# Kernel optimization log

Measured on AMD Instinct MI355X. Metric: run time of the kernel, lower is better.

The kernel has to match this reference:

```python
import jax, jax.numpy as jnp
import numpy as np

NUM_HEADS = 16
EPS = 1e-06


def setup_inputs() -> dict:
    key = jax.random.key(0)
    ks = jax.random.split(key, 6)
    b, s, d = 4, 4096, 1024
    scale = 1.0 / np.sqrt(d)
    return {
        "x": jax.random.normal(ks[0], (b, s, d), dtype=jnp.float32),
        "wq": jax.random.normal(ks[1], (d, d), dtype=jnp.float32) * scale,
        "wk": jax.random.normal(ks[2], (d, d), dtype=jnp.float32) * scale,
        "wv": jax.random.normal(ks[3], (d, d), dtype=jnp.float32) * scale,
        "wo": jax.random.normal(ks[4], (d, d), dtype=jnp.float32) * scale,
        "bo": jnp.zeros((d,), dtype=jnp.float32),
    }


def _split_heads(t, h):
    b, s, d = t.shape
    return t.reshape(b, s, h, d // h).transpose(0, 2, 1, 3)  # [b,h,s,dh]


def reference(x, wq, wk, wv, wo, bo):
    h = NUM_HEADS
    # torch Linear: y = x @ W.T (no bias for q/k/v)
    q = _split_heads(x @ wq.T, h)
    k = _split_heads(x @ wk.T, h)
    v = _split_heads(x @ wv.T, h)
    # ELU+1 feature map
    qf = jax.nn.elu(q) + 1.0
    kf = jax.nn.elu(k) + 1.0
    # global key feature sum over sequence: [b,h,dh]
    k_sum = jnp.sum(kf, axis=-2)
    # denominator: [b,h,s,1]
    denom = jnp.sum(qf * k_sum[:, :, None, :], axis=-1, keepdims=True) + EPS
    # kv = sum_s kf_s (outer) v_s  -> [b,h,dh,dh]  (the broadcast-sum in torch == matmul)
    kv = jnp.einsum('bhsd,bhse->bhde', kf, v)
    # q_kv: [b,h,s,dh]
    q_kv = jnp.einsum('bhsd,bhde->bhse', qf, kv)
    out = q_kv / denom
    b, _, s, dh = out.shape
    out = out.transpose(0, 2, 1, 3).reshape(b, s, h * dh)  # merge heads
    return out @ wo.T + bo
```

## Files before the change

kernel.cpp:

```cpp
#include <hip/hip_runtime.h>
#include <hip/hip_bf16.h>
#include <cmath>


#define TOK    16384
#define DMODEL 1024
#define NHEAD  16
#define DH     64
#define KSPLIT 8

using bf16x8 = __attribute__((ext_vector_type(8))) short;
using f32x4  = __attribute__((ext_vector_type(4))) float;

typedef __attribute__((address_space(1))) const unsigned int gld_src_t;
typedef __attribute__((address_space(3))) unsigned int gld_dst_t;

__device__ __forceinline__ unsigned short f2bf(float x) {
    unsigned int u = __float_as_uint(x);
    u += 0x7fffu + ((u >> 16) & 1u);
    return (unsigned short)(u >> 16);
}
__device__ __forceinline__ float bf2f(unsigned short b) {
    return __uint_as_float((unsigned int)b << 16);
}

__global__ __launch_bounds__(256) void split_k(
    const float* __restrict__ in, unsigned short* __restrict__ hi,
    unsigned short* __restrict__ lo, int n)
{
    int i = (blockIdx.x * 256 + threadIdx.x) * 4;
    if (i >= n) return;
    float4 v = *(const float4*)(in + i);
    float vs[4] = {v.x, v.y, v.z, v.w};
    unsigned short hh[4], ll[4];
#pragma unroll
    for (int j = 0; j < 4; ++j) {
        unsigned short h = f2bf(vs[j]);
        hh[j] = h;
        ll[j] = f2bf(vs[j] - bf2f(h));
    }
    *(ushort4*)(hi + i) = make_ushort4(hh[0], hh[1], hh[2], hh[3]);
    *(ushort4*)(lo + i) = make_ushort4(ll[0], ll[1], ll[2], ll[3]);
}

__global__ __launch_bounds__(256) void splitw_k(
    const float* __restrict__ w0, const float* __restrict__ w1,
    const float* __restrict__ w2, const float* __restrict__ w3,
    unsigned short* __restrict__ hs, unsigned short* __restrict__ ls)
{
    int w = blockIdx.x >> 10;
    const float* src = (w == 0) ? w0 : (w == 1) ? w1 : (w == 2) ? w2 : w3;
    int i = ((blockIdx.x & 1023) * 256 + threadIdx.x) * 4;
    size_t base = (size_t)w * (DMODEL * DMODEL);
    float4 v = *(const float4*)(src + i);
    float vs[4] = {v.x, v.y, v.z, v.w};
    unsigned short hh[4], ll[4];
#pragma unroll
    for (int j = 0; j < 4; ++j) {
        unsigned short h = f2bf(vs[j]);
        hh[j] = h;
        ll[j] = f2bf(vs[j] - bf2f(h));
    }
    *(ushort4*)(hs + base + i) = make_ushort4(hh[0], hh[1], hh[2], hh[3]);
    *(ushort4*)(ls + base + i) = make_ushort4(ll[0], ll[1], ll[2], ll[3]);
}

template<int ACT>
__global__ __launch_bounds__(512, 2) void gemm256_k(
    const unsigned short* __restrict__ Ah, const unsigned short* __restrict__ Al,
    const unsigned short* __restrict__ Bh, const unsigned short* __restrict__ Bl,
    const float* __restrict__ bias, float* __restrict__ C,
    int M, int N, int K)
{
    __shared__ unsigned short lds[2][4][256 * 32];
    const int tid  = threadIdx.x;
    const int lane = tid & 63, wid = tid >> 6;

    const int nwg = gridDim.x, cpx = nwg >> 3;
    const int g = ((int)blockIdx.x & 7) * cpx + ((int)blockIdx.x >> 3);
    const int m0 = (g >> 2) * 256, n0 = (g & 3) * 256;

    const int wr = wid >> 2, wc = wid & 3;
    const int fr = lane & 15, ko = lane >> 4;

    f32x4 acc[8][4];
#pragma unroll
    for (int i = 0; i < 8; ++i)
#pragma unroll
        for (int j = 0; j < 4; ++j) acc[i][j] = (f32x4){0.f, 0.f, 0.f, 0.f};

    const unsigned short* srcb = (wid < 2) ? Ah : (wid < 4) ? Al : (wid < 6) ? Bh : Bl;
    const int rowbase = ((wid < 4) ? m0 : n0) + (wid & 1) * 128;
    const int rloc = (wid & 1) * 128 + (lane >> 2);
    const int sslot = (lane & 3) ^ ((rloc >> 1) & 3);
    const unsigned short* gsrc0 = srcb + (size_t)(rowbase + (lane >> 2)) * K + sslot * 8;
    const int mat  = wid >> 1;
    const int ldso = ((wid & 1) * 128) * 32;

    const int koff = (ko ^ ((fr >> 1) & 3)) * 8;

    const int nt = K / 32;

#pragma unroll
    for (int t = 0; t < 8; ++t) {
        __builtin_amdgcn_global_load_lds((gld_src_t*)(gsrc0 + (size_t)t * 16 * K),
            (gld_dst_t*)&lds[0][mat][ldso + t * 512], 16, 0, 0);
    }
    __syncthreads();

    for (int t = 0; t < nt; ++t) {
        const int cur = t & 1;
        if (t + 1 < nt) {
            const unsigned short* gk = gsrc0 + (size_t)(t + 1) * 32;
#pragma unroll
            for (int u = 0; u < 8; ++u) {
                __builtin_amdgcn_global_load_lds((gld_src_t*)(gk + (size_t)u * 16 * K),
                    (gld_dst_t*)&lds[cur ^ 1][mat][ldso + u * 512], 16, 0, 0);
            }
        }
        bf16x8 ah[8], al[8];
#pragma unroll
        for (int mi = 0; mi < 8; ++mi) {
            int off = (wr * 128 + mi * 16 + fr) * 32 + koff;
            ah[mi] = *(const bf16x8*)&lds[cur][0][off];
            al[mi] = *(const bf16x8*)&lds[cur][1][off];
        }
#pragma unroll
        for (int nj = 0; nj < 4; ++nj) {
            int off = (wc * 64 + nj * 16 + fr) * 32 + koff;
            bf16x8 bh = *(const bf16x8*)&lds[cur][2][off];
            bf16x8 bl = *(const bf16x8*)&lds[cur][3][off];
#pragma unroll
            for (int mi = 0; mi < 8; ++mi) {
                acc[mi][nj] = __builtin_amdgcn_mfma_f32_16x16x32_bf16(ah[mi], bh, acc[mi][nj], 0, 0, 0);
                acc[mi][nj] = __builtin_amdgcn_mfma_f32_16x16x32_bf16(ah[mi], bl, acc[mi][nj], 0, 0, 0);
                acc[mi][nj] = __builtin_amdgcn_mfma_f32_16x16x32_bf16(al[mi], bh, acc[mi][nj], 0, 0, 0);
            }
        }
        __syncthreads();
    }

    const int fq = ko;
#pragma unroll
    for (int mi = 0; mi < 8; ++mi) {
#pragma unroll
        for (int i = 0; i < 4; ++i) {
            int m = m0 + wr * 128 + mi * 16 + fq * 4 + i;
            float* crow = C + (size_t)m * N + n0 + wc * 64;
#pragma unroll
            for (int nj = 0; nj < 4; ++nj) {
                int n = nj * 16 + fr;
                float v = acc[mi][nj][i];
                if (ACT == 1) v = (v > 0.f) ? (v + 1.f) : expf(v);
                if (ACT == 2) v += bias[n0 + wc * 64 + n];
                crow[n] = v;
            }
        }
    }
}

__global__ __launch_bounds__(256) void kv_partial_k(
    const float* __restrict__ kf, const float* __restrict__ vchunk,
    int bh_base, float* __restrict__ kvp, float* __restrict__ ksp)
{
    __shared__ float kfs[8][64];
    __shared__ float vs[8][64];
    const int bh = bh_base + blockIdx.x;
    const int split = blockIdx.y;
    const int b = bh >> 4, h = bh & 15;
    const int blocal = b - (bh_base >> 4);
    const int tid = threadIdx.x;
    const int col = tid & 63, rg = tid >> 6;
    const int tx = tid & 15, ty = tid >> 4;
    const int di0 = ty * 4, dj0 = tx * 4;

    float acc[4][4] = {};
    float ks[4] = {0.f, 0.f, 0.f, 0.f};

    const int rows = 4096 / KSPLIT;
    const size_t kbase = ((size_t)b * 4096 + (size_t)split * rows) * DMODEL + h * DH;
    const size_t vbase = ((size_t)blocal * 4096 + (size_t)split * rows) * DMODEL + h * DH;

    for (int it = 0; it < rows / 8; ++it) {
        __syncthreads();
#pragma unroll
        for (int p = 0; p < 2; ++p) {
            int r = rg + p * 4;
            size_t o = (size_t)(it * 8 + r) * DMODEL + col;
            kfs[r][col] = kf[kbase + o];
            vs[r][col]  = vchunk[vbase + o];
        }
        __syncthreads();
#pragma unroll
        for (int r = 0; r < 8; ++r) {
            float a[4], bb[4];
#pragma unroll
            for (int i = 0; i < 4; ++i) a[i] = kfs[r][di0 + i];
#pragma unroll
            for (int j = 0; j < 4; ++j) bb[j] = vs[r][dj0 + j];
#pragma unroll
            for (int i = 0; i < 4; ++i)
#pragma unroll
                for (int j = 0; j < 4; ++j)
                    acc[i][j] = fmaf(a[i], bb[j], acc[i][j]);
            if (tx == 0) {
#pragma unroll
                for (int i = 0; i < 4; ++i) ks[i] += a[i];
            }
        }
    }

    const size_t obase = ((size_t)(bh * KSPLIT + split)) * (DH * DH);
#pragma unroll
    for (int i = 0; i < 4; ++i)
#pragma unroll
        for (int j = 0; j < 4; ++j)
            kvp[obase + (size_t)(di0 + i) * DH + dj0 + j] = acc[i][j];
    if (tx == 0) {
        size_t kb = ((size_t)(bh * KSPLIT + split)) * DH + di0;
#pragma unroll
        for (int i = 0; i < 4; ++i) ksp[kb + i] = ks[i];
    }
}

__global__ __launch_bounds__(256) void reduce_kv_k(
    const float* __restrict__ kvp, const float* __restrict__ ksp,
    float* __restrict__ kv, float* __restrict__ ksum)
{
    int idx = blockIdx.x * 256 + threadIdx.x;
    int bh = idx >> 12, off = idx & 4095;
    float s = 0.f;
    for (int c = 0; c < KSPLIT; ++c) s += kvp[((size_t)(bh * KSPLIT + c)) * 4096 + off];
    kv[idx] = s;
    if (idx < 64 * DH) {
        int bh2 = idx >> 6, o2 = idx & 63;
        float t = 0.f;
        for (int c = 0; c < KSPLIT; ++c) t += ksp[((size_t)(bh2 * KSPLIT + c)) * DH + o2];
        ksum[idx] = t;
    }
}

__global__ __launch_bounds__(256) void attn_out_k(
    const float* __restrict__ qf_in, const float* __restrict__ kv,
    const float* __restrict__ ksum, unsigned short* __restrict__ out_hi,
    unsigned short* __restrict__ out_lo)
{
    __shared__ float kvs[DH * DH];
    __shared__ float qfs[16][DH];
    __shared__ float ksums[DH];
    __shared__ float denoms[16];
    const int hh = blockIdx.y;
    const int t0 = blockIdx.x * 16;
    const int b = t0 >> 12;
    const int bh = b * NHEAD + hh;
    const int tid = threadIdx.x;

    for (int i = tid; i < DH * DH; i += 256) kvs[i] = kv[(size_t)bh * (DH * DH) + i];
    for (int i = tid; i < 16 * DH; i += 256) {
        int tok = i >> 6, e = i & 63;
        qfs[tok][e] = qf_in[(size_t)(t0 + tok) * DMODEL + hh * DH + e];
    }
    if (tid < DH) ksums[tid] = ksum[(size_t)bh * DH + tid];
    __syncthreads();
    if (tid < 16) {
        float d = 0.f;
#pragma unroll
        for (int i = 0; i < DH; ++i) d += qfs[tid][i] * ksums[i];
        denoms[tid] = d + 1e-6f;
    }
    __syncthreads();
#pragma unroll
    for (int k = 0; k < 4; ++k) {
        int o = tid + k * 256;
        int tok = o >> 6, e = o & 63;
        float s = 0.f;
#pragma unroll
        for (int d = 0; d < DH; ++d) s = fmaf(qfs[tok][d], kvs[d * DH + e], s);
        s /= denoms[tok];
        size_t idx = (size_t)(t0 + tok) * DMODEL + hh * DH + e;
        unsigned short hb = f2bf(s);
        out_hi[idx] = hb;
        out_lo[idx] = f2bf(s - bf2f(hb));
    }
}

extern "C" void kernel_launch(void* const* d_in, const int* in_sizes, int n_in,
                              void* d_out, int out_size, void* d_ws, size_t ws_size,
                              hipStream_t stream)
{
    const float* x  = (const float*)d_in[0];
    const float* wq = (const float*)d_in[1];
    const float* wk = (const float*)d_in[2];
    const float* wv = (const float*)d_in[3];
    const float* wo = (const float*)d_in[4];
    const float* bo = (const float*)d_in[5];
    float* out = (float*)d_out;

    const size_t XE = (size_t)TOK * DMODEL;
    const size_t WE = (size_t)DMODEL * DMODEL;
    const size_t CE = (size_t)8192 * DMODEL;

    unsigned short* xh = (unsigned short*)d_ws;
    unsigned short* xl = xh + XE;
    unsigned short* wh = xl + XE;
    unsigned short* wl = wh + 4 * WE;
    float* kf   = (float*)(wl + 4 * WE);
    float* vc   = kf + XE;
    float* kvp  = vc + CE;
    float* ksp  = kvp + (size_t)64 * KSPLIT * DH * DH;
    float* kvb  = ksp + (size_t)64 * KSPLIT * DH;
    float* ksmb = kvb + (size_t)64 * DH * DH;
    float* qf   = kf;

    split_k<<<(int)(XE / 1024), 256, 0, stream>>>(x, xh, xl, (int)XE);
    splitw_k<<<4096, 256, 0, stream>>>(wq, wk, wv, wo, wh, wl);

    const int gfull = (TOK / 256) * 4;
    const int ghalf = (8192 / 256) * 4;

    gemm256_k<1><<<gfull, 512, 0, stream>>>(xh, xl, wh + WE, wl + WE, nullptr, kf, TOK, DMODEL, DMODEL);

    gemm256_k<0><<<ghalf, 512, 0, stream>>>(xh, xl, wh + 2 * WE, wl + 2 * WE, nullptr, vc, 8192, DMODEL, DMODEL);
    kv_partial_k<<<dim3(32, KSPLIT), 256, 0, stream>>>(kf, vc, 0, kvp, ksp);

    gemm256_k<0><<<ghalf, 512, 0, stream>>>(xh + CE, xl + CE, wh + 2 * WE, wl + 2 * WE, nullptr, vc, 8192, DMODEL, DMODEL);
    kv_partial_k<<<dim3(32, KSPLIT), 256, 0, stream>>>(kf, vc, 32, kvp, ksp);

    reduce_kv_k<<<dim3(64 * DH * DH / 256), 256, 0, stream>>>(kvp, ksp, kvb, ksmb);

    gemm256_k<1><<<gfull, 512, 0, stream>>>(xh, xl, wh, wl, nullptr, qf, TOK, DMODEL, DMODEL);
    attn_out_k<<<dim3(TOK / 16, NHEAD), 256, 0, stream>>>(qf, kvb, ksmb, xh, xl);

    gemm256_k<2><<<gfull, 512, 0, stream>>>(xh, xl, wh + 3 * WE, wl + 3 * WE, bo, out, TOK, DMODEL, DMODEL);
}
```

Baseline: 585.0 us.

## Compute attention output with split-bf16 MFMA, folding denominator into augmented KV

The Q projection GEMM now writes its feature-mapped output directly as hi/lo bf16 pairs instead of fp32. The KV reduction emits a transposed, bf16-split KV matrix with k_sum appended as extra rows. A new MFMA-based attention kernel then computes q·kv and the denominator in one pass of 3-term split-bf16 matrix products. This replaces the scalar fp32 FMA attention kernel and halves the Q intermediate traffic, at the cost of bf16x3 rounding in the attention step and some padding rows in the KV tile.

New measurement: 523.7 us, median of 2. 1.12x faster.

```diff
diff --git a/kernel.cpp b/kernel.cpp
--- a/kernel.cpp
+++ b/kernel.cpp
@@ -70,6 +70,7 @@
     const unsigned short* __restrict__ Ah, const unsigned short* __restrict__ Al,
     const unsigned short* __restrict__ Bh, const unsigned short* __restrict__ Bl,
     const float* __restrict__ bias, float* __restrict__ C,
+    unsigned short* __restrict__ Ch, unsigned short* __restrict__ Cl,
     int M, int N, int K)
 {
     __shared__ unsigned short lds[2][4][256 * 32];
@@ -98,7 +99,6 @@
     const int ldso = ((wid & 1) * 128) * 32;
 
     const int koff = (ko ^ ((fr >> 1) & 3)) * 8;
-
     const int nt = K / 32;
 
 #pragma unroll
@@ -146,14 +146,20 @@
 #pragma unroll
         for (int i = 0; i < 4; ++i) {
             int m = m0 + wr * 128 + mi * 16 + fq * 4 + i;
-            float* crow = C + (size_t)m * N + n0 + wc * 64;
+            size_t rbase = (size_t)m * N + n0 + wc * 64;
 #pragma unroll
             for (int nj = 0; nj < 4; ++nj) {
                 int n = nj * 16 + fr;
                 float v = acc[mi][nj][i];
-                if (ACT == 1) v = (v > 0.f) ? (v + 1.f) : expf(v);
+                if (ACT == 1 || ACT == 3) v = (v > 0.f) ? (v + 1.f) : expf(v);
                 if (ACT == 2) v += bias[n0 + wc * 64 + n];
-                crow[n] = v;
+                if (ACT == 3) {
+                    unsigned short hb = f2bf(v);
+                    Ch[rbase + n] = hb;
+                    Cl[rbase + n] = f2bf(v - bf2f(hb));
+                } else {
+                    C[rbase + n] = v;
+                }
             }
         }
     }
@@ -225,62 +231,107 @@
 
 __global__ __launch_bounds__(256) void reduce_kv_k(
     const float* __restrict__ kvp, const float* __restrict__ ksp,
-    float* __restrict__ kv, float* __restrict__ ksum)
+    unsigned short* __restrict__ kvth, unsigned short* __restrict__ kvtl)
 {
     int idx = blockIdx.x * 256 + threadIdx.x;
     int bh = idx >> 12, off = idx & 4095;
+    int d = off & 63, e = off >> 6;
     float s = 0.f;
-    for (int c = 0; c < KSPLIT; ++c) s += kvp[((size_t)(bh * KSPLIT + c)) * 4096 + off];
-    kv[idx] = s;
+    for (int c = 0; c < KSPLIT; ++c) s += kvp[((size_t)(bh * KSPLIT + c)) * 4096 + d * 64 + e];
+    unsigned short hb = f2bf(s);
+    size_t o = (size_t)bh * (96 * 64) + (size_t)e * 64 + d;
+    kvth[o] = hb;
+    kvtl[o] = f2bf(s - bf2f(hb));
     if (idx < 64 * DH) {
-        int bh2 = idx >> 6, o2 = idx & 63;
+        int bh2 = idx >> 6, d2 = idx & 63;
         float t = 0.f;
-        for (int c = 0; c < KSPLIT; ++c) t += ksp[((size_t)(bh2 * KSPLIT + c)) * DH + o2];
-        ksum[idx] = t;
-    }
-}
-
-__global__ __launch_bounds__(256) void attn_out_k(
-    const float* __restrict__ qf_in, const float* __restrict__ kv,
-    const float* __restrict__ ksum, unsigned short* __restrict__ out_hi,
-    unsigned short* __restrict__ out_lo)
-{
-    __shared__ float kvs[DH * DH];
-    __shared__ float qfs[16][DH];
-    __shared__ float ksums[DH];
-    __shared__ float denoms[16];
-    const int hh = blockIdx.y;
-    const int t0 = blockIdx.x * 16;
-    const int b = t0 >> 12;
-    const int bh = b * NHEAD + hh;
-    const int tid = threadIdx.x;
-
-    for (int i = tid; i < DH * DH; i += 256) kvs[i] = kv[(size_t)bh * (DH * DH) + i];
-    for (int i = tid; i < 16 * DH; i += 256) {
-        int tok = i >> 6, e = i & 63;
-        qfs[tok][e] = qf_in[(size_t)(t0 + tok) * DMODEL + hh * DH + e];
-    }
-    if (tid < DH) ksums[tid] = ksum[(size_t)bh * DH + tid];
+        for (int c = 0; c < KSPLIT; ++c) t += ksp[((size_t)(bh2 * KSPLIT + c)) * DH + d2];
+        unsigned short h2 = f2bf(t);
+        size_t o2 = (size_t)bh2 * (96 * 64) + 64 * 64 + d2;
+        kvth[o2] = h2;
+        kvtl[o2] = f2bf(t - bf2f(h2));
+    }
+}
+
+__global__ __launch_bounds__(512, 2) void attn_mfma_k(
+    const unsigned short* __restrict__ qh, const unsigned short* __restrict__ ql,
+    const unsigned short* __restrict__ kvth, const unsigned short* __restrict__ kvtl,
+    unsigned short* __restrict__ out_hi, unsigned short* __restrict__ out_lo)
+{
+    __shared__ unsigned short lds[28672];
+    __shared__ float denoms[128];
+    const int tid = threadIdx.x, lane = tid & 63, wid = tid >> 6;
+    const int blk = blockIdx.x;
+    const int bh = blk >> 5, tb = blk & 31;
+    const int b = bh >> 4, h = bh & 15;
+    const int t0 = b * 4096 + tb * 128;
+
+    const int l8 = lane >> 3, s7 = lane & 7;
+#pragma unroll
+    for (int shot = 0; shot < 7; ++shot) {
+        int r = wid * 7 + shot;
+        const unsigned short* src;
+        int dstE;
+        if (r < 32) {
+            int row = (r & 15) * 8 + l8;
+            int sslot = s7 ^ (row & 7);
+            src = ((r < 16) ? qh : ql) + (size_t)(t0 + row) * DMODEL + h * DH + sslot * 8;
+            dstE = ((r < 16) ? 0 : 8192) + (r & 15) * 512;
+        } else {
+            int rb = r - 32;
+            int rl = (rb < 12) ? rb : rb - 12;
+            int row = rl * 8 + l8;
+            int sslot = s7 ^ (row & 7);
+            src = ((rb < 12) ? kvth : kvtl) + (size_t)bh * (96 * 64) + row * 64 + sslot * 8;
+            dstE = ((rb < 12) ? 16384 : 22528) + rl * 512;
+        }
+        __builtin_amdgcn_global_load_lds((gld_src_t*)src, (gld_dst_t*)&lds[dstE], 16, 0, 0);
+    }
     __syncthreads();
-    if (tid < 16) {
-        float d = 0.f;
-#pragma unroll
-        for (int i = 0; i < DH; ++i) d += qfs[tid][i] * ksums[i];
-        denoms[tid] = d + 1e-6f;
+
+    const int fr = lane & 15, ko = lane >> 4, fq = ko;
+    const int arow = wid * 16 + fr;
+
+    f32x4 acc[5];
+#pragma unroll
+    for (int nj = 0; nj < 5; ++nj) acc[nj] = (f32x4){0.f, 0.f, 0.f, 0.f};
+
+#pragma unroll
+    for (int kt = 0; kt < 2; ++kt) {
+        int aoff = arow * 64 + ((kt * 4 + ko) ^ (arow & 7)) * 8;
+        bf16x8 a_h = *(const bf16x8*)&lds[aoff];
+        bf16x8 a_l = *(const bf16x8*)&lds[8192 + aoff];
+#pragma unroll
+        for (int nj = 0; nj < 5; ++nj) {
+            int brow = nj * 16 + fr;
+            int boff = brow * 64 + ((kt * 4 + ko) ^ (brow & 7)) * 8;
+            bf16x8 b_h = *(const bf16x8*)&lds[16384 + boff];
+            bf16x8 b_l = *(const bf16x8*)&lds[22528 + boff];
+            acc[nj] = __builtin_amdgcn_mfma_f32_16x16x32_bf16(a_h, b_h, acc[nj], 0, 0, 0);
+            acc[nj] = __builtin_amdgcn_mfma_f32_16x16x32_bf16(a_h, b_l, acc[nj], 0, 0, 0);
+            acc[nj] = __builtin_amdgcn_mfma_f32_16x16x32_bf16(a_l, b_h, acc[nj], 0, 0, 0);
+        }
+    }
+
+    if (fr == 0) {
+#pragma unroll
+        for (int i = 0; i < 4; ++i)
+            denoms[wid * 16 + fq * 4 + i] = acc[4][i] + 1e-6f;
     }
     __syncthreads();
-#pragma unroll
-    for (int k = 0; k < 4; ++k) {
-        int o = tid + k * 256;
-        int tok = o >> 6, e = o & 63;
-        float s = 0.f;
-#pragma unroll
-        for (int d = 0; d < DH; ++d) s = fmaf(qfs[tok][d], kvs[d * DH + e], s);
-        s /= denoms[tok];
-        size_t idx = (size_t)(t0 + tok) * DMODEL + hh * DH + e;
-        unsigned short hb = f2bf(s);
-        out_hi[idx] = hb;
-        out_lo[idx] = f2bf(s - bf2f(hb));
+
+#pragma unroll
+    for (int i = 0; i < 4; ++i) {
+        int row = wid * 16 + fq * 4 + i;
+        float dinv = 1.0f / denoms[row];
+        size_t rbase = (size_t)(t0 + row) * DMODEL + h * DH;
+#pragma unroll
+        for (int nj = 0; nj < 4; ++nj) {
+            float v = acc[nj][i] * dinv;
+            unsigned short hb = f2bf(v);
+            out_hi[rbase + nj * 16 + fr] = hb;
+            out_lo[rbase + nj * 16 + fr] = f2bf(v - bf2f(hb));
+        }
     }
 }
 
@@ -308,9 +359,10 @@
     float* vc   = kf + XE;
     float* kvp  = vc + CE;
     float* ksp  = kvp + (size_t)64 * KSPLIT * DH * DH;
-    float* kvb  = ksp + (size_t)64 * KSPLIT * DH;
-    float* ksmb = kvb + (size_t)64 * DH * DH;
-    float* qf   = kf;
+    unsigned short* kvth = (unsigned short*)(ksp + (size_t)64 * KSPLIT * DH);
+    unsigned short* kvtl = kvth + (size_t)64 * 96 * 64;
+    unsigned short* qh = (unsigned short*)kf;
+    unsigned short* ql = qh + XE;
 
     split_k<<<(int)(XE / 1024), 256, 0, stream>>>(x, xh, xl, (int)XE);
     splitw_k<<<4096, 256, 0, stream>>>(wq, wk, wv, wo, wh, wl);
@@ -318,18 +370,18 @@
     const int gfull = (TOK / 256) * 4;
     const int ghalf = (8192 / 256) * 4;
 
-    gemm256_k<1><<<gfull, 512, 0, stream>>>(xh, xl, wh + WE, wl + WE, nullptr, kf, TOK, DMODEL, DMODEL);
-
-    gemm256_k<0><<<ghalf, 512, 0, stream>>>(xh, xl, wh + 2 * WE, wl + 2 * WE, nullptr, vc, 8192, DMODEL, DMODEL);
+    gemm256_k<1><<<gfull, 512, 0, stream>>>(xh, xl, wh + WE, wl + WE, nullptr, kf, nullptr, nullptr, TOK, DMODEL, DMODEL);
+
+    gemm256_k<0><<<ghalf, 512, 0, stream>>>(xh, xl, wh + 2 * WE, wl + 2 * WE, nullptr, vc, nullptr, nullptr, 8192, DMODEL, DMODEL);
     kv_partial_k<<<dim3(32, KSPLIT), 256, 0, stream>>>(kf, vc, 0, kvp, ksp);
 
-    gemm256_k<0><<<ghalf, 512, 0, stream>>>(xh + CE, xl + CE, wh + 2 * WE, wl + 2 * WE, nullptr, vc, 8192, DMODEL, DMODEL);
+    gemm256_k<0><<<ghalf, 512, 0, stream>>>(xh + CE, xl + CE, wh + 2 * WE, wl + 2 * WE, nullptr, vc, nullptr, nullptr, 8192, DMODEL, DMODEL);
     kv_partial_k<<<dim3(32, KSPLIT), 256, 0, stream>>>(kf, vc, 32, kvp, ksp);
 
-    reduce_kv_k<<<dim3(64 * DH * DH / 256), 256, 0, stream>>>(kvp, ksp, kvb, ksmb);
-
-    gemm256_k<1><<<gfull, 512, 0, stream>>>(xh, xl, wh, wl, nullptr, qf, TOK, DMODEL, DMODEL);
-    attn_out_k<<<dim3(TOK / 16, NHEAD), 256, 0, stream>>>(qf, kvb, ksmb, xh, xl);
-
-    gemm256_k<2><<<gfull, 512, 0, stream>>>(xh, xl, wh + 3 * WE, wl + 3 * WE, bo, out, TOK, DMODEL, DMODEL);
-}
+    reduce_kv_k<<<dim3(64 * DH * DH / 256), 256, 0, stream>>>(kvp, ksp, kvth, kvtl);
+
+    gemm256_k<3><<<gfull, 512, 0, stream>>>(xh, xl, wh, wl, nullptr, nullptr, qh, ql, TOK, DMODEL, DMODEL);
+    attn_mfma_k<<<2048, 512, 0, stream>>>(qh, ql, kvth, kvtl, xh, xl);
+
+    gemm256_k<2><<<gfull, 512, 0, stream>>>(xh, xl, wh + 3 * WE, wl + 3 * WE, bo, out, nullptr, nullptr, TOK, DMODEL, DMODEL);
+}
```
